# Optimization experiments

Measured on AMD Instinct MI355X. Metric: run time of the kernel, lower is better.

## Reference

```python
import jax, jax.numpy as jnp
import numpy as np

B, H, T, DH = 2, 16, 2048, 64
SCALE = DH ** -0.5


def setup_inputs() -> dict:
    key = jax.random.key(0)
    kq, kk, kv = jax.random.split(key, 3)
    q = jax.random.normal(kq, (B, H, T, DH), dtype=jnp.float32)
    k = jax.random.normal(kk, (B, H, T, DH), dtype=jnp.float32)
    v = jax.random.normal(kv, (B, H, T, DH), dtype=jnp.float32)
    attention_mask = jnp.ones((B, T), dtype=bool)  # (B, Tk) padding mask, True=keep
    causal_mask = jnp.tril(jnp.ones((T, T), dtype=bool))[None, None]  # (1,1,Tq,Tk)
    return {"q": q, "k": k, "v": v, "attention_mask": attention_mask,
            "causal_mask": causal_mask}


def _attend(q, k, v, attention_mask, causal_mask):
    # scores in fp32 as in the torch module
    scores = jnp.einsum("bhqd,bhkd->bhqk", q.astype(jnp.float32),
                        k.astype(jnp.float32)) * SCALE
    neg_inf = jnp.float32(-jnp.inf)
    # (B,Tk) bool padding mask -> (B,1,1,Tk), broadcasts over Tq
    pad = attention_mask[:, None, None, :]
    scores = jnp.where(pad, scores, neg_inf)
    scores = jnp.where(causal_mask, scores, neg_inf)
    attn = jax.nn.softmax(scores, axis=-1).astype(q.dtype)
    ctx = jnp.einsum("bhqk,bhkd->bhqd", attn, v)  # (B,H,Tq,Dh)
    Bq, Hq, Tq, Dh = ctx.shape
    return ctx.transpose(0, 2, 1, 3).reshape(Bq, Tq, Hq * Dh)


def reference(q, k, v, attention_mask, causal_mask):
    return _attend(q, k, v, attention_mask, causal_mask)
```

## Files before the change

### kernel.cpp

```cpp
#include <hip/hip_runtime.h>


constexpr int Bc = 2, Hc = 16, Tc = 2048, Dc = 64;
constexpr float QSCALE = 0.125f * 1.44269504088896340736f;

typedef __attribute__((__ext_vector_type__(8))) __bf16 bf16x8;
typedef __attribute__((__ext_vector_type__(4))) __bf16 bf16x4;
typedef __attribute__((__ext_vector_type__(4))) float f32x4;

__global__ __launch_bounds__(256, 4) void attn_fwd_kernel(
    const float* __restrict__ Q,
    const float* __restrict__ K,
    const float* __restrict__ V,
    float* __restrict__ O)
{
  const int tid  = threadIdx.x;
  const int wave = tid >> 6;
  const int lane = tid & 63;
  const int l16  = lane & 15;
  const int g    = lane >> 4;

  const int bid   = blockIdx.x;
  const int head  = bid & 31;
  const int qtile = 31 - (bid >> 5);
  const int b = head >> 4, h = head & 15;
  const int q0 = qtile * 64 + wave * 16;

  const size_t hoff = (size_t)head * Tc * Dc;
  const float* Qb = Q + hoff;
  const float* Kb = K + hoff;
  const float* Vb = V + hoff;

  __shared__ __bf16 Kl[2][64 * 64];
  __shared__ __bf16 Vt[2][64 * 64];

  const int krow = tid >> 2;
  const int seg  = tid & 3;
  const int kswz = (krow & 7) << 4;
  const int vkb  = tid >> 4;
  const int vdb  = tid & 15;
  const int vwx  = (vdb >> 2) << 3;

  bf16x8 qf[2];
  {
    const float4* qp = (const float4*)(Qb + (size_t)(q0 + l16) * Dc + g * 8);
    #pragma unroll
    for (int c = 0; c < 2; ++c) {
      float4 x0 = qp[c * 8], x1 = qp[c * 8 + 1];
      const float* f0 = (const float*)&x0;
      const float* f1 = (const float*)&x1;
      #pragma unroll
      for (int j = 0; j < 4; ++j) {
        qf[c][j]     = (__bf16)(f0[j] * QSCALE);
        qf[c][4 + j] = (__bf16)(f1[j] * QSCALE);
      }
    }
  }

  f32x4 o_acc[4] = {};
  float m_run = -1e30f;
  float l_part = 0.f;
  const int n_iter = qtile + 1;
  float4 kreg[4], vreg[4];

  {
    const float4* kp4 = (const float4*)(Kb + (size_t)krow * Dc + seg * 16);
    #pragma unroll
    for (int c = 0; c < 4; ++c) kreg[c] = kp4[c];
    const float* vb0 = Vb + (size_t)(vkb * 4) * Dc + vdb * 4;
    #pragma unroll
    for (int r = 0; r < 4; ++r) vreg[r] = *(const float4*)(vb0 + r * Dc);

    #pragma unroll
    for (int hh = 0; hh < 2; ++hh) {
      const float* x0 = (const float*)&kreg[2 * hh];
      const float* x1 = (const float*)&kreg[2 * hh + 1];
      bf16x8 t;
      #pragma unroll
      for (int j = 0; j < 4; ++j) { t[j] = (__bf16)x0[j]; t[4 + j] = (__bf16)x1[j]; }
      *(bf16x8*)((char*)Kl[0] + krow * 128 + ((seg * 32 + hh * 16) ^ kswz)) = t;
    }
    #pragma unroll
    for (int i = 0; i < 4; ++i) {
      bf16x4 t;
      #pragma unroll
      for (int r = 0; r < 4; ++r) t[r] = (__bf16)((const float*)&vreg[r])[i];
      const int d = vdb * 4 + i;
      *(bf16x4*)((char*)Vt[0] + vkb * 512 + ((d * 8) ^ (vkb << 3) ^ vwx)) = t;
    }
  }

  for (int it = 0; it < n_iter; ++it) {
    __syncthreads();
    const int cur = it & 1;

    const bool more = (it + 1 < n_iter);
    if (more) {
      const int kv1 = (it + 1) * 64;
      const float4* kp4 = (const float4*)(Kb + (size_t)(kv1 + krow) * Dc + seg * 16);
      #pragma unroll
      for (int c = 0; c < 4; ++c) kreg[c] = kp4[c];
      const float* vb0 = Vb + (size_t)(kv1 + vkb * 4) * Dc + vdb * 4;
      #pragma unroll
      for (int r = 0; r < 4; ++r) vreg[r] = *(const float4*)(vb0 + r * Dc);
    }

    const bool partial = (it == qtile);
    const int  ns = partial ? (wave + 1) : 4;

    f32x4 sacc[4];
    __builtin_amdgcn_s_setprio(1);
    #pragma unroll
    for (int s = 0; s < 4; ++s) {
      if (s < ns) {
        f32x4 z = {0.f, 0.f, 0.f, 0.f};
        const int row = s * 16 + l16;
        const char* kb = (const char*)Kl[cur] + row * 128;
        const int swz = (row & 7) << 4;
        bf16x8 k0 = *(const bf16x8*)(kb + ((g * 16) ^ swz));
        bf16x8 k1 = *(const bf16x8*)(kb + ((64 + g * 16) ^ swz));
        z = __builtin_amdgcn_mfma_f32_16x16x32_bf16(k0, qf[0], z, 0, 0, 0);
        z = __builtin_amdgcn_mfma_f32_16x16x32_bf16(k1, qf[1], z, 0, 0, 0);
        sacc[s] = z;
      } else {
        sacc[s] = f32x4{-INFINITY, -INFINITY, -INFINITY, -INFINITY};
      }
    }
    __builtin_amdgcn_s_setprio(0);
    if (partial) {
      #pragma unroll
      for (int s = 0; s < 4; ++s)
        #pragma unroll
        for (int r = 0; r < 4; ++r)
          if (s * 16 + g * 4 + r > wave * 16 + l16) sacc[s][r] = -INFINITY;
    }

    float v16[16];
    #pragma unroll
    for (int s = 0; s < 4; ++s)
      #pragma unroll
      for (int r = 0; r < 4; ++r) v16[s * 4 + r] = sacc[s][r];
    #pragma unroll
    for (int w = 8; w >= 1; w >>= 1)
      #pragma unroll
      for (int i = 0; i < 8; ++i)
        if (i < w) v16[i] = fmaxf(v16[i], v16[i + w]);
    const float mxl = v16[0];

    if (!__all(mxl <= m_run + 8.0f)) {
      float mx = fmaxf(mxl, __shfl_xor(mxl, 16, 64));
      mx = fmaxf(mx, __shfl_xor(mx, 32, 64));
      const float mn = fmaxf(m_run, mx);
      const float f  = __builtin_amdgcn_exp2f(m_run - mn);
      m_run = mn;
      l_part *= f;
      #pragma unroll
      for (int r = 0; r < 4; ++r) {
        const float fo = __shfl(f, g * 4 + r, 64);
        #pragma unroll
        for (int dt = 0; dt < 4; ++dt) o_acc[dt][r] *= fo;
      }
    }

    float pv16[16];
    bf16x8 pa[2];
    #pragma unroll
    for (int c = 0; c < 2; ++c)
      #pragma unroll
      for (int j = 0; j < 8; ++j) {
        const float pv = __builtin_amdgcn_exp2f(sacc[2 * c + (j >> 2)][j & 3] - m_run);
        pv16[c * 8 + j] = pv;
        pa[c][j] = (__bf16)pv;
      }
    #pragma unroll
    for (int w = 8; w >= 1; w >>= 1)
      #pragma unroll
      for (int i = 0; i < 8; ++i)
        if (i < w) pv16[i] += pv16[i + w];
    l_part += pv16[0];

    __builtin_amdgcn_s_setprio(1);
    #pragma unroll
    for (int dt = 0; dt < 4; ++dt) {
      const int d = dt * 16 + l16;
      const int dx = (dt & 3) << 3;
      #pragma unroll
      for (int c = 0; c < 2; ++c) {
        const int kc0 = 8 * c + g;
        const int kc1 = 8 * c + 4 + g;
        union { bf16x8 v8; bf16x4 v4[2]; } uu;
        uu.v4[0] = *(const bf16x4*)((char*)Vt[cur] + kc0 * 512 + ((d * 8) ^ (kc0 << 3) ^ dx));
        uu.v4[1] = *(const bf16x4*)((char*)Vt[cur] + kc1 * 512 + ((d * 8) ^ (kc1 << 3) ^ dx));
        o_acc[dt] = __builtin_amdgcn_mfma_f32_16x16x32_bf16(pa[c], uu.v8, o_acc[dt], 0, 0, 0);
      }
    }
    __builtin_amdgcn_s_setprio(0);

    if (more) {
      const int nxt = cur ^ 1;
      #pragma unroll
      for (int hh = 0; hh < 2; ++hh) {
        const float* x0 = (const float*)&kreg[2 * hh];
        const float* x1 = (const float*)&kreg[2 * hh + 1];
        bf16x8 t;
        #pragma unroll
        for (int j = 0; j < 4; ++j) { t[j] = (__bf16)x0[j]; t[4 + j] = (__bf16)x1[j]; }
        *(bf16x8*)((char*)Kl[nxt] + krow * 128 + ((seg * 32 + hh * 16) ^ kswz)) = t;
      }
      #pragma unroll
      for (int i = 0; i < 4; ++i) {
        bf16x4 t;
        #pragma unroll
        for (int r = 0; r < 4; ++r) t[r] = (__bf16)((const float*)&vreg[r])[i];
        const int d = vdb * 4 + i;
        *(bf16x4*)((char*)Vt[nxt] + vkb * 512 + ((d * 8) ^ (vkb << 3) ^ vwx)) = t;
      }
    }
  }

  float l_run = l_part;
  l_run += __shfl_xor(l_run, 16, 64);
  l_run += __shfl_xor(l_run, 32, 64);

  #pragma unroll
  for (int r = 0; r < 4; ++r) {
    const float il = __shfl(l_run, g * 4 + r, 64);
    const float inv = 1.f / il;
    float* orow = O + ((size_t)b * Tc + (q0 + g * 4 + r)) * (Hc * Dc) + h * Dc;
    #pragma unroll
    for (int dt = 0; dt < 4; ++dt)
      orow[dt * 16 + l16] = o_acc[dt][r] * inv;
  }
}

extern "C" void kernel_launch(void* const* d_in, const int* in_sizes, int n_in,
                              void* d_out, int out_size, void* d_ws, size_t ws_size,
                              hipStream_t stream) {
  const float* q = (const float*)d_in[0];
  const float* k = (const float*)d_in[1];
  const float* v = (const float*)d_in[2];
  float* out = (float*)d_out;

  dim3 grid(1024);
  dim3 block(256);
  hipLaunchKernelGGL(attn_fwd_kernel, grid, block, 0, stream, q, k, v, out);
}
```

Measured before the change: 55.72 us.

## Split query tiles to 32 rows with 2-wave blocks and double grid

Each block now handles 32 query rows with two waves instead of 64 rows with four, doubling the grid to 2048 blocks. Each thread loads twice as much K/V into shared memory per 64-key tile, and the causal partial-tile logic is generalised to the new offsets. The row max and sum reductions across lane groups are now done every iteration instead of once at the end. The intent is finer causal work granularity and better load balance across CUs, at the cost of each K/V tile being loaded by twice as many blocks and extra per-iteration shuffles.

```diff
diff --git a/kernel.cpp b/kernel.cpp
--- a/kernel.cpp
+++ b/kernel.cpp
@@ -8,7 +8,7 @@
 typedef __attribute__((__ext_vector_type__(4))) __bf16 bf16x4;
 typedef __attribute__((__ext_vector_type__(4))) float f32x4;
 
-__global__ __launch_bounds__(256, 4) void attn_fwd_kernel(
+__global__ __launch_bounds__(128, 3) void attn_fwd_kernel(
     const float* __restrict__ Q,
     const float* __restrict__ K,
     const float* __restrict__ V,
@@ -20,24 +20,25 @@
   const int l16  = lane & 15;
   const int g    = lane >> 4;
 
-  const int bid   = blockIdx.x;
-  const int head  = bid & 31;
-  const int qtile = 31 - (bid >> 5);
+  const int bid  = blockIdx.x;
+  const int head = bid & 31;
+  const int h32  = 63 - (bid >> 5);
   const int b = head >> 4, h = head & 15;
-  const int q0 = qtile * 64 + wave * 16;
+  const int q0 = h32 * 32 + wave * 16;
+  const int n_iter = (h32 >> 1) + 1;
 
   const size_t hoff = (size_t)head * Tc * Dc;
   const float* Qb = Q + hoff;
   const float* Kb = K + hoff;
   const float* Vb = V + hoff;
 
-  __shared__ __bf16 Kl[2][64 * 64];
-  __shared__ __bf16 Vt[2][64 * 64];
-
-  const int krow = tid >> 2;
-  const int seg  = tid & 3;
+  __shared__ __bf16 Kl[2][4096];
+  __shared__ __bf16 Vt[2][4096];
+
+  const int krow = tid >> 1;
+  const int seg  = tid & 1;
   const int kswz = (krow & 7) << 4;
-  const int vkb  = tid >> 4;
+  const int vkb0 = tid >> 4;
   const int vdb  = tid & 15;
   const int vwx  = (vdb >> 2) << 3;
 
@@ -58,35 +59,43 @@
   }
 
   f32x4 o_acc[4] = {};
-  float m_run = -1e30f;
-  float l_part = 0.f;
-  const int n_iter = qtile + 1;
-  float4 kreg[4], vreg[4];
+  float m_run = -1e30f, l_run = 0.f;
+
+  float4 kreg[8];
+  float4 vreg[2][4];
 
   {
-    const float4* kp4 = (const float4*)(Kb + (size_t)krow * Dc + seg * 16);
-    #pragma unroll
-    for (int c = 0; c < 4; ++c) kreg[c] = kp4[c];
-    const float* vb0 = Vb + (size_t)(vkb * 4) * Dc + vdb * 4;
-    #pragma unroll
-    for (int r = 0; r < 4; ++r) vreg[r] = *(const float4*)(vb0 + r * Dc);
-
-    #pragma unroll
-    for (int hh = 0; hh < 2; ++hh) {
-      const float* x0 = (const float*)&kreg[2 * hh];
-      const float* x1 = (const float*)&kreg[2 * hh + 1];
+    const float4* kp4 = (const float4*)(Kb + (size_t)krow * Dc + seg * 32);
+    #pragma unroll
+    for (int c = 0; c < 8; ++c) kreg[c] = kp4[c];
+    #pragma unroll
+    for (int kci = 0; kci < 2; ++kci) {
+      const int kc = vkb0 + 8 * kci;
+      const float* vb0 = Vb + (size_t)(kc * 4) * Dc + vdb * 4;
+      #pragma unroll
+      for (int rr = 0; rr < 4; ++rr) vreg[kci][rr] = *(const float4*)(vb0 + rr * Dc);
+    }
+
+    #pragma unroll
+    for (int cc = 0; cc < 4; ++cc) {
+      const float* x0 = (const float*)&kreg[2 * cc];
+      const float* x1 = (const float*)&kreg[2 * cc + 1];
       bf16x8 t;
       #pragma unroll
       for (int j = 0; j < 4; ++j) { t[j] = (__bf16)x0[j]; t[4 + j] = (__bf16)x1[j]; }
-      *(bf16x8*)((char*)Kl[0] + krow * 128 + ((seg * 32 + hh * 16) ^ kswz)) = t;
-    }
-    #pragma unroll
-    for (int i = 0; i < 4; ++i) {
-      bf16x4 t;
-      #pragma unroll
-      for (int r = 0; r < 4; ++r) t[r] = (__bf16)((const float*)&vreg[r])[i];
-      const int d = vdb * 4 + i;
-      *(bf16x4*)((char*)Vt[0] + vkb * 512 + ((d * 8) ^ (vkb << 3) ^ vwx)) = t;
+      *(bf16x8*)((char*)Kl[0] + krow * 128 + ((seg * 64 + cc * 16) ^ kswz)) = t;
+    }
+    #pragma unroll
+    for (int kci = 0; kci < 2; ++kci) {
+      const int kc = vkb0 + 8 * kci;
+      #pragma unroll
+      for (int i = 0; i < 4; ++i) {
+        bf16x4 t;
+        #pragma unroll
+        for (int rr = 0; rr < 4; ++rr) t[rr] = (__bf16)((const float*)&vreg[kci][rr])[i];
+        const int d = vdb * 4 + i;
+        *(bf16x4*)((char*)Vt[0] + kc * 512 + ((d * 8) ^ (kc << 3) ^ vwx)) = t;
+      }
     }
   }
 
@@ -97,16 +106,20 @@
     const bool more = (it + 1 < n_iter);
     if (more) {
       const int kv1 = (it + 1) * 64;
-      const float4* kp4 = (const float4*)(Kb + (size_t)(kv1 + krow) * Dc + seg * 16);
-      #pragma unroll
-      for (int c = 0; c < 4; ++c) kreg[c] = kp4[c];
-      const float* vb0 = Vb + (size_t)(kv1 + vkb * 4) * Dc + vdb * 4;
-      #pragma unroll
-      for (int r = 0; r < 4; ++r) vreg[r] = *(const float4*)(vb0 + r * Dc);
-    }
-
-    const bool partial = (it == qtile);
-    const int  ns = partial ? (wave + 1) : 4;
+      const float4* kp4 = (const float4*)(Kb + (size_t)(kv1 + krow) * Dc + seg * 32);
+      #pragma unroll
+      for (int c = 0; c < 8; ++c) kreg[c] = kp4[c];
+      #pragma unroll
+      for (int kci = 0; kci < 2; ++kci) {
+        const int kc = vkb0 + 8 * kci;
+        const float* vb0 = Vb + (size_t)(kv1 + kc * 4) * Dc + vdb * 4;
+        #pragma unroll
+        for (int rr = 0; rr < 4; ++rr) vreg[kci][rr] = *(const float4*)(vb0 + rr * Dc);
+      }
+    }
+
+    const bool partial = (it == n_iter - 1);
+    const int  ns = partial ? (((q0 + 15 - it * 64) >> 4) + 1) : 4;
 
     f32x4 sacc[4];
     __builtin_amdgcn_s_setprio(1);
@@ -128,11 +141,12 @@
     }
     __builtin_amdgcn_s_setprio(0);
     if (partial) {
+      const int qrel = q0 + l16 - it * 64;
       #pragma unroll
       for (int s = 0; s < 4; ++s)
         #pragma unroll
         for (int r = 0; r < 4; ++r)
-          if (s * 16 + g * 4 + r > wave * 16 + l16) sacc[s][r] = -INFINITY;
+          if (s * 16 + g * 4 + r > qrel) sacc[s][r] = -INFINITY;
     }
 
     float v16[16];
@@ -145,15 +159,15 @@
       #pragma unroll
       for (int i = 0; i < 8; ++i)
         if (i < w) v16[i] = fmaxf(v16[i], v16[i + w]);
-    const float mxl = v16[0];
-
-    if (!__all(mxl <= m_run + 8.0f)) {
-      float mx = fmaxf(mxl, __shfl_xor(mxl, 16, 64));
-      mx = fmaxf(mx, __shfl_xor(mx, 32, 64));
+    float mx = v16[0];
+    mx = fmaxf(mx, __shfl_xor(mx, 16, 64));
+    mx = fmaxf(mx, __shfl_xor(mx, 32, 64));
+
+    if (!__all(mx <= m_run + 8.0f)) {
       const float mn = fmaxf(m_run, mx);
       const float f  = __builtin_amdgcn_exp2f(m_run - mn);
       m_run = mn;
-      l_part *= f;
+      l_run *= f;
       #pragma unroll
       for (int r = 0; r < 4; ++r) {
         const float fo = __shfl(f, g * 4 + r, 64);
@@ -177,7 +191,10 @@
       #pragma unroll
       for (int i = 0; i < 8; ++i)
         if (i < w) pv16[i] += pv16[i + w];
-    l_part += pv16[0];
+    float sum = pv16[0];
+    sum += __shfl_xor(sum, 16, 64);
+    sum += __shfl_xor(sum, 32, 64);
+    l_run += sum;
 
     __builtin_amdgcn_s_setprio(1);
     #pragma unroll
@@ -199,28 +216,28 @@
     if (more) {
       const int nxt = cur ^ 1;
       #pragma unroll
-      for (int hh = 0; hh < 2; ++hh) {
-        const float* x0 = (const float*)&kreg[2 * hh];
-        const float* x1 = (const float*)&kreg[2 * hh + 1];
+      for (int cc = 0; cc < 4; ++cc) {
+        const float* x0 = (const float*)&kreg[2 * cc];
+        const float* x1 = (const float*)&kreg[2 * cc + 1];
         bf16x8 t;
         #pragma unroll
         for (int j = 0; j < 4; ++j) { t[j] = (__bf16)x0[j]; t[4 + j] = (__bf16)x1[j]; }
-        *(bf16x8*)((char*)Kl[nxt] + krow * 128 + ((seg * 32 + hh * 16) ^ kswz)) = t;
-      }
-      #pragma unroll
-      for (int i = 0; i < 4; ++i) {
-        bf16x4 t;
-        #pragma unroll
-        for (int r = 0; r < 4; ++r) t[r] = (__bf16)((const float*)&vreg[r])[i];
-        const int d = vdb * 4 + i;
-        *(bf16x4*)((char*)Vt[nxt] + vkb * 512 + ((d * 8) ^ (vkb << 3) ^ vwx)) = t;
-      }
-    }
-  }
-
-  float l_run = l_part;
-  l_run += __shfl_xor(l_run, 16, 64);
-  l_run += __shfl_xor(l_run, 32, 64);
+        *(bf16x8*)((char*)Kl[nxt] + krow * 128 + ((seg * 64 + cc * 16) ^ kswz)) = t;
+      }
+      #pragma unroll
+      for (int kci = 0; kci < 2; ++kci) {
+        const int kc = vkb0 + 8 * kci;
+        #pragma unroll
+        for (int i = 0; i < 4; ++i) {
+          bf16x4 t;
+          #pragma unroll
+          for (int rr = 0; rr < 4; ++rr) t[rr] = (__bf16)((const float*)&vreg[kci][rr])[i];
+          const int d = vdb * 4 + i;
+          *(bf16x4*)((char*)Vt[nxt] + kc * 512 + ((d * 8) ^ (kc << 3) ^ vwx)) = t;
+        }
+      }
+    }
+  }
 
   #pragma unroll
   for (int r = 0; r < 4; ++r) {
@@ -241,7 +258,7 @@
   const float* v = (const float*)d_in[2];
   float* out = (float*)d_out;
 
-  dim3 grid(1024);
-  dim3 block(256);
+  dim3 grid(2048);
+  dim3 block(128);
   hipLaunchKernelGGL(attn_fwd_kernel, grid, block, 0, stream, q, k, v, out);
 }
```

New measurement: 104.3 us. 1.87x slower.

## Use 128-row query tiles with 8 waves sharing each K/V tile load

Applied to the files above, without the earlier changes.

Doubles the query tile per block to 128 rows (8 waves, 512 threads) and halves the grid, so each staged K/V tile in shared memory serves twice as many queries. K and V staging is split across thread halves: the first 256 threads load K, the rest load V and transpose it. Waves whose rows lie entirely above the diagonal for a given KV tile skip that tile's compute. The row-sum reduction now happens every iteration. The change cuts global K/V traffic and per-thread staging registers, but leaves fewer blocks for load balancing, idles some waves on diagonal tiles, and adds cross-lane shuffles per iteration.

```diff
diff --git a/kernel.cpp b/kernel.cpp
--- a/kernel.cpp
+++ b/kernel.cpp
@@ -8,7 +8,7 @@
 typedef __attribute__((__ext_vector_type__(4))) __bf16 bf16x4;
 typedef __attribute__((__ext_vector_type__(4))) float f32x4;
 
-__global__ __launch_bounds__(256, 4) void attn_fwd_kernel(
+__global__ __launch_bounds__(512, 4) void attn_fwd_kernel(
     const float* __restrict__ Q,
     const float* __restrict__ K,
     const float* __restrict__ V,
@@ -22,23 +22,26 @@
 
   const int bid   = blockIdx.x;
   const int head  = bid & 31;
-  const int qtile = 31 - (bid >> 5);
+  const int qtile = 15 - (bid >> 5);
   const int b = head >> 4, h = head & 15;
-  const int q0 = qtile * 64 + wave * 16;
+  const int q0 = qtile * 128 + wave * 16;
+  const int n_iter = 2 * qtile + 2;
 
   const size_t hoff = (size_t)head * Tc * Dc;
   const float* Qb = Q + hoff;
   const float* Kb = K + hoff;
   const float* Vb = V + hoff;
 
-  __shared__ __bf16 Kl[2][64 * 64];
-  __shared__ __bf16 Vt[2][64 * 64];
-
-  const int krow = tid >> 2;
-  const int seg  = tid & 3;
+  __shared__ __bf16 Kl[2][4096];
+  __shared__ __bf16 Vt[2][4096];
+
+  const bool doK = (tid < 256);
+  const int t2   = tid & 255;
+  const int krow = t2 >> 2;
+  const int seg  = t2 & 3;
   const int kswz = (krow & 7) << 4;
-  const int vkb  = tid >> 4;
-  const int vdb  = tid & 15;
+  const int vkb  = t2 >> 4;
+  const int vdb  = t2 & 15;
   const int vwx  = (vdb >> 2) << 3;
 
   bf16x8 qf[2];
@@ -58,35 +61,35 @@
   }
 
   f32x4 o_acc[4] = {};
-  float m_run = -1e30f;
-  float l_part = 0.f;
-  const int n_iter = qtile + 1;
-  float4 kreg[4], vreg[4];
+  float m_run = -1e30f, l_run = 0.f;
+  float4 sreg[4];
 
   {
-    const float4* kp4 = (const float4*)(Kb + (size_t)krow * Dc + seg * 16);
-    #pragma unroll
-    for (int c = 0; c < 4; ++c) kreg[c] = kp4[c];
-    const float* vb0 = Vb + (size_t)(vkb * 4) * Dc + vdb * 4;
-    #pragma unroll
-    for (int r = 0; r < 4; ++r) vreg[r] = *(const float4*)(vb0 + r * Dc);
-
-    #pragma unroll
-    for (int hh = 0; hh < 2; ++hh) {
-      const float* x0 = (const float*)&kreg[2 * hh];
-      const float* x1 = (const float*)&kreg[2 * hh + 1];
-      bf16x8 t;
-      #pragma unroll
-      for (int j = 0; j < 4; ++j) { t[j] = (__bf16)x0[j]; t[4 + j] = (__bf16)x1[j]; }
-      *(bf16x8*)((char*)Kl[0] + krow * 128 + ((seg * 32 + hh * 16) ^ kswz)) = t;
-    }
-    #pragma unroll
-    for (int i = 0; i < 4; ++i) {
-      bf16x4 t;
-      #pragma unroll
-      for (int r = 0; r < 4; ++r) t[r] = (__bf16)((const float*)&vreg[r])[i];
-      const int d = vdb * 4 + i;
-      *(bf16x4*)((char*)Vt[0] + vkb * 512 + ((d * 8) ^ (vkb << 3) ^ vwx)) = t;
+    if (doK) {
+      const float4* kp4 = (const float4*)(Kb + (size_t)krow * Dc + seg * 16);
+      #pragma unroll
+      for (int c = 0; c < 4; ++c) sreg[c] = kp4[c];
+      #pragma unroll
+      for (int hh = 0; hh < 2; ++hh) {
+        const float* x0 = (const float*)&sreg[2 * hh];
+        const float* x1 = (const float*)&sreg[2 * hh + 1];
+        bf16x8 t;
+        #pragma unroll
+        for (int j = 0; j < 4; ++j) { t[j] = (__bf16)x0[j]; t[4 + j] = (__bf16)x1[j]; }
+        *(bf16x8*)((char*)Kl[0] + krow * 128 + ((seg * 32 + hh * 16) ^ kswz)) = t;
+      }
+    } else {
+      const float* vb0 = Vb + (size_t)(vkb * 4) * Dc + vdb * 4;
+      #pragma unroll
+      for (int r = 0; r < 4; ++r) sreg[r] = *(const float4*)(vb0 + r * Dc);
+      #pragma unroll
+      for (int i = 0; i < 4; ++i) {
+        bf16x4 t;
+        #pragma unroll
+        for (int r = 0; r < 4; ++r) t[r] = (__bf16)((const float*)&sreg[r])[i];
+        const int d = vdb * 4 + i;
+        *(bf16x4*)((char*)Vt[0] + vkb * 512 + ((d * 8) ^ (vkb << 3) ^ vwx)) = t;
+      }
     }
   }
 
@@ -97,130 +100,138 @@
     const bool more = (it + 1 < n_iter);
     if (more) {
       const int kv1 = (it + 1) * 64;
-      const float4* kp4 = (const float4*)(Kb + (size_t)(kv1 + krow) * Dc + seg * 16);
-      #pragma unroll
-      for (int c = 0; c < 4; ++c) kreg[c] = kp4[c];
-      const float* vb0 = Vb + (size_t)(kv1 + vkb * 4) * Dc + vdb * 4;
-      #pragma unroll
-      for (int r = 0; r < 4; ++r) vreg[r] = *(const float4*)(vb0 + r * Dc);
-    }
-
-    const bool partial = (it == qtile);
-    const int  ns = partial ? (wave + 1) : 4;
-
-    f32x4 sacc[4];
-    __builtin_amdgcn_s_setprio(1);
-    #pragma unroll
-    for (int s = 0; s < 4; ++s) {
-      if (s < ns) {
-        f32x4 z = {0.f, 0.f, 0.f, 0.f};
-        const int row = s * 16 + l16;
-        const char* kb = (const char*)Kl[cur] + row * 128;
-        const int swz = (row & 7) << 4;
-        bf16x8 k0 = *(const bf16x8*)(kb + ((g * 16) ^ swz));
-        bf16x8 k1 = *(const bf16x8*)(kb + ((64 + g * 16) ^ swz));
-        z = __builtin_amdgcn_mfma_f32_16x16x32_bf16(k0, qf[0], z, 0, 0, 0);
-        z = __builtin_amdgcn_mfma_f32_16x16x32_bf16(k1, qf[1], z, 0, 0, 0);
-        sacc[s] = z;
+      if (doK) {
+        const float4* kp4 = (const float4*)(Kb + (size_t)(kv1 + krow) * Dc + seg * 16);
+        #pragma unroll
+        for (int c = 0; c < 4; ++c) sreg[c] = kp4[c];
       } else {
-        sacc[s] = f32x4{-INFINITY, -INFINITY, -INFINITY, -INFINITY};
-      }
-    }
-    __builtin_amdgcn_s_setprio(0);
-    if (partial) {
+        const float* vb0 = Vb + (size_t)(kv1 + vkb * 4) * Dc + vdb * 4;
+        #pragma unroll
+        for (int r = 0; r < 4; ++r) sreg[r] = *(const float4*)(vb0 + r * Dc);
+      }
+    }
+
+    const int qrel = q0 + 15 - it * 64;
+    const int nsr  = (qrel >> 4) + 1;
+    const int ns   = nsr < 0 ? 0 : (nsr > 4 ? 4 : nsr);
+
+    if (ns > 0) {
+      f32x4 sacc[4];
+      __builtin_amdgcn_s_setprio(1);
+      #pragma unroll
+      for (int s = 0; s < 4; ++s) {
+        if (s < ns) {
+          f32x4 z = {0.f, 0.f, 0.f, 0.f};
+          const int row = s * 16 + l16;
+          const char* kb = (const char*)Kl[cur] + row * 128;
+          const int swz = (row & 7) << 4;
+          bf16x8 k0 = *(const bf16x8*)(kb + ((g * 16) ^ swz));
+          bf16x8 k1 = *(const bf16x8*)(kb + ((64 + g * 16) ^ swz));
+          z = __builtin_amdgcn_mfma_f32_16x16x32_bf16(k0, qf[0], z, 0, 0, 0);
+          z = __builtin_amdgcn_mfma_f32_16x16x32_bf16(k1, qf[1], z, 0, 0, 0);
+          sacc[s] = z;
+        } else {
+          sacc[s] = f32x4{-INFINITY, -INFINITY, -INFINITY, -INFINITY};
+        }
+      }
+      __builtin_amdgcn_s_setprio(0);
+      if (it * 64 + 63 > q0) {
+        #pragma unroll
+        for (int s = 0; s < 4; ++s)
+          #pragma unroll
+          for (int r = 0; r < 4; ++r)
+            if (it * 64 + s * 16 + g * 4 + r > q0 + l16) sacc[s][r] = -INFINITY;
+      }
+
+      float v16[16];
       #pragma unroll
       for (int s = 0; s < 4; ++s)
         #pragma unroll
-        for (int r = 0; r < 4; ++r)
-          if (s * 16 + g * 4 + r > wave * 16 + l16) sacc[s][r] = -INFINITY;
-    }
-
-    float v16[16];
-    #pragma unroll
-    for (int s = 0; s < 4; ++s)
-      #pragma unroll
-      for (int r = 0; r < 4; ++r) v16[s * 4 + r] = sacc[s][r];
-    #pragma unroll
-    for (int w = 8; w >= 1; w >>= 1)
-      #pragma unroll
-      for (int i = 0; i < 8; ++i)
-        if (i < w) v16[i] = fmaxf(v16[i], v16[i + w]);
-    const float mxl = v16[0];
-
-    if (!__all(mxl <= m_run + 8.0f)) {
-      float mx = fmaxf(mxl, __shfl_xor(mxl, 16, 64));
+        for (int r = 0; r < 4; ++r) v16[s * 4 + r] = sacc[s][r];
+      #pragma unroll
+      for (int w = 8; w >= 1; w >>= 1)
+        #pragma unroll
+        for (int i = 0; i < 8; ++i)
+          if (i < w) v16[i] = fmaxf(v16[i], v16[i + w]);
+      float mx = v16[0];
+      mx = fmaxf(mx, __shfl_xor(mx, 16, 64));
       mx = fmaxf(mx, __shfl_xor(mx, 32, 64));
-      const float mn = fmaxf(m_run, mx);
-      const float f  = __builtin_amdgcn_exp2f(m_run - mn);
-      m_run = mn;
-      l_part *= f;
-      #pragma unroll
-      for (int r = 0; r < 4; ++r) {
-        const float fo = __shfl(f, g * 4 + r, 64);
-        #pragma unroll
-        for (int dt = 0; dt < 4; ++dt) o_acc[dt][r] *= fo;
-      }
-    }
-
-    float pv16[16];
-    bf16x8 pa[2];
-    #pragma unroll
-    for (int c = 0; c < 2; ++c)
-      #pragma unroll
-      for (int j = 0; j < 8; ++j) {
-        const float pv = __builtin_amdgcn_exp2f(sacc[2 * c + (j >> 2)][j & 3] - m_run);
-        pv16[c * 8 + j] = pv;
-        pa[c][j] = (__bf16)pv;
-      }
-    #pragma unroll
-    for (int w = 8; w >= 1; w >>= 1)
-      #pragma unroll
-      for (int i = 0; i < 8; ++i)
-        if (i < w) pv16[i] += pv16[i + w];
-    l_part += pv16[0];
-
-    __builtin_amdgcn_s_setprio(1);
-    #pragma unroll
-    for (int dt = 0; dt < 4; ++dt) {
-      const int d = dt * 16 + l16;
-      const int dx = (dt & 3) << 3;
-      #pragma unroll
-      for (int c = 0; c < 2; ++c) {
-        const int kc0 = 8 * c + g;
-        const int kc1 = 8 * c + 4 + g;
-        union { bf16x8 v8; bf16x4 v4[2]; } uu;
-        uu.v4[0] = *(const bf16x4*)((char*)Vt[cur] + kc0 * 512 + ((d * 8) ^ (kc0 << 3) ^ dx));
-        uu.v4[1] = *(const bf16x4*)((char*)Vt[cur] + kc1 * 512 + ((d * 8) ^ (kc1 << 3) ^ dx));
-        o_acc[dt] = __builtin_amdgcn_mfma_f32_16x16x32_bf16(pa[c], uu.v8, o_acc[dt], 0, 0, 0);
-      }
-    }
-    __builtin_amdgcn_s_setprio(0);
+
+      if (!__all(mx <= m_run + 8.0f)) {
+        const float mn = fmaxf(m_run, mx);
+        const float f  = __builtin_amdgcn_exp2f(m_run - mn);
+        m_run = mn;
+        l_run *= f;
+        #pragma unroll
+        for (int r = 0; r < 4; ++r) {
+          const float fo = __shfl(f, g * 4 + r, 64);
+          #pragma unroll
+          for (int dt = 0; dt < 4; ++dt) o_acc[dt][r] *= fo;
+        }
+      }
+
+      float pv16[16];
+      bf16x8 pa[2];
+      #pragma unroll
+      for (int c = 0; c < 2; ++c)
+        #pragma unroll
+        for (int j = 0; j < 8; ++j) {
+          const float pv = __builtin_amdgcn_exp2f(sacc[2 * c + (j >> 2)][j & 3] - m_run);
+          pv16[c * 8 + j] = pv;
+          pa[c][j] = (__bf16)pv;
+        }
+      #pragma unroll
+      for (int w = 8; w >= 1; w >>= 1)
+        #pragma unroll
+        for (int i = 0; i < 8; ++i)
+          if (i < w) pv16[i] += pv16[i + w];
+      float sum = pv16[0];
+      sum += __shfl_xor(sum, 16, 64);
+      sum += __shfl_xor(sum, 32, 64);
+      l_run += sum;
+
+      __builtin_amdgcn_s_setprio(1);
+      #pragma unroll
+      for (int dt = 0; dt < 4; ++dt) {
+        const int d = dt * 16 + l16;
+        const int dx = (dt & 3) << 3;
+        #pragma unroll
+        for (int c = 0; c < 2; ++c) {
+          const int kc0 = 8 * c + g;
+          const int kc1 = 8 * c + 4 + g;
+          union { bf16x8 v8; bf16x4 v4[2]; } uu;
+          uu.v4[0] = *(const bf16x4*)((char*)Vt[cur] + kc0 * 512 + ((d * 8) ^ (kc0 << 3) ^ dx));
+          uu.v4[1] = *(const bf16x4*)((char*)Vt[cur] + kc1 * 512 + ((d * 8) ^ (kc1 << 3) ^ dx));
+          o_acc[dt] = __builtin_amdgcn_mfma_f32_16x16x32_bf16(pa[c], uu.v8, o_acc[dt], 0, 0, 0);
+        }
+      }
+      __builtin_amdgcn_s_setprio(0);
+    }
 
     if (more) {
       const int nxt = cur ^ 1;
-      #pragma unroll
-      for (int hh = 0; hh < 2; ++hh) {
-        const float* x0 = (const float*)&kreg[2 * hh];
-        const float* x1 = (const float*)&kreg[2 * hh + 1];
-        bf16x8 t;
-        #pragma unroll
-        for (int j = 0; j < 4; ++j) { t[j] = (__bf16)x0[j]; t[4 + j] = (__bf16)x1[j]; }
-        *(bf16x8*)((char*)Kl[nxt] + krow * 128 + ((seg * 32 + hh * 16) ^ kswz)) = t;
-      }
-      #pragma unroll
-      for (int i = 0; i < 4; ++i) {
-        bf16x4 t;
-        #pragma unroll
-        for (int r = 0; r < 4; ++r) t[r] = (__bf16)((const float*)&vreg[r])[i];
-        const int d = vdb * 4 + i;
-        *(bf16x4*)((char*)Vt[nxt] + vkb * 512 + ((d * 8) ^ (vkb << 3) ^ vwx)) = t;
-      }
-    }
-  }
-
-  float l_run = l_part;
-  l_run += __shfl_xor(l_run, 16, 64);
-  l_run += __shfl_xor(l_run, 32, 64);
+      if (doK) {
+        #pragma unroll
+        for (int hh = 0; hh < 2; ++hh) {
+          const float* x0 = (const float*)&sreg[2 * hh];
+          const float* x1 = (const float*)&sreg[2 * hh + 1];
+          bf16x8 t;
+          #pragma unroll
+          for (int j = 0; j < 4; ++j) { t[j] = (__bf16)x0[j]; t[4 + j] = (__bf16)x1[j]; }
+          *(bf16x8*)((char*)Kl[nxt] + krow * 128 + ((seg * 32 + hh * 16) ^ kswz)) = t;
+        }
+      } else {
+        #pragma unroll
+        for (int i = 0; i < 4; ++i) {
+          bf16x4 t;
+          #pragma unroll
+          for (int r = 0; r < 4; ++r) t[r] = (__bf16)((const float*)&sreg[r])[i];
+          const int d = vdb * 4 + i;
+          *(bf16x4*)((char*)Vt[nxt] + vkb * 512 + ((d * 8) ^ (vkb << 3) ^ vwx)) = t;
+        }
+      }
+    }
+  }
 
   #pragma unroll
   for (int r = 0; r < 4; ++r) {
@@ -241,7 +252,7 @@
   const float* v = (const float*)d_in[2];
   float* out = (float*)d_out;
 
-  dim3 grid(1024);
-  dim3 block(256);
+  dim3 grid(512);
+  dim3 block(512);
   hipLaunchKernelGGL(attn_fwd_kernel, grid, block, 0, stream, q, k, v, out);
 }
```

Result: slower. 136.6 us (+145.2%).
